# Optimization experiments

Measured on AMD Instinct MI355X. Metric: run time of the kernel, lower is better.

Reference implementation:

```python
import jax, jax.numpy as jnp
import numpy as np
import math

N_NODES = 100000
N_EDGES = 3200000
F_IN = 512
HID = 128
N_CLS = 16


def setup_inputs() -> dict:
    key = jax.random.key(0)
    k = jax.random.split(key, 6)
    x = jax.random.normal(k[0], (N_NODES, F_IN), dtype=jnp.float32)
    edge_index = jax.random.randint(k[1], (2, N_EDGES), 0, N_NODES, dtype=jnp.int32)
    W1 = jax.random.normal(k[2], (F_IN, HID), dtype=jnp.float32) / np.sqrt(F_IN)
    W2 = jax.random.normal(k[3], (HID, HID), dtype=jnp.float32) / np.sqrt(HID)
    W3 = jax.random.normal(k[4], (N_CLS, HID), dtype=jnp.float32) / np.sqrt(HID)
    b3 = jnp.zeros((N_CLS,), dtype=jnp.float32)
    return {"x": x, "edge_index": edge_index, "W1": W1, "W2": W2, "W3": W3, "b3": b3}


def _sym_norm(edge_index, num_nodes, dtype):
    # add self loops with fill_value = trunc(log2(average_node_degree))
    E = edge_index.shape[1]
    fill = float(math.trunc(math.log2(E / num_nodes)))
    loops = jnp.arange(num_nodes, dtype=edge_index.dtype)
    row = jnp.concatenate([edge_index[0], loops])
    col = jnp.concatenate([edge_index[1], loops])
    w = jnp.concatenate([jnp.ones((E,), dtype), jnp.full((num_nodes,), fill, dtype)])
    deg = jax.ops.segment_sum(w, row, num_segments=num_nodes)
    deg_inv_sqrt = jnp.where(deg > 0, jax.lax.rsqrt(deg), 0.0)
    norm = deg_inv_sqrt[row] * w * deg_inv_sqrt[col]
    return row, col, norm


def reference(x, edge_index, W1, W2, W3, b3):
    N = x.shape[0]
    row, col, norm = _sym_norm(edge_index, N, x.dtype)

    def gcn(h, W):
        h = h @ W                                   # [N, d_out]
        msg = norm[:, None] * h[col]                # gather + scale, [E', d_out]
        return jax.ops.segment_sum(msg, row, num_segments=N)

    h = jax.nn.relu(gcn(x, W1))      # layer 1 + srelu (threshold clamped at 0)
    h = gcn(h, W2)                   # layer 2
    # dropout p=0.5 is identity in eval mode
    return h @ W3.T + b3             # linear classifier [N, n_classes]
```

## Files before the change

kernel.cpp:

```cpp
#include <hip/hip_runtime.h>
#include <cmath>

typedef __attribute__((ext_vector_type(8))) short short8;
typedef __attribute__((ext_vector_type(8))) unsigned short ushort8;
typedef __attribute__((ext_vector_type(4))) float f32x4;
typedef __attribute__((ext_vector_type(4))) unsigned int uint4v;

#define EPB 4096

__device__ inline float bf16_lo(unsigned int p) {
  union { unsigned int i; float f; } v; v.i = p << 16; return v.f;
}
__device__ inline float bf16_hi(unsigned int p) {
  union { unsigned int i; float f; } v; v.i = p & 0xffff0000u; return v.f;
}
__device__ inline unsigned short f32_to_bf16(float f) {
  union { float f; unsigned int i; } v; v.f = f;
  unsigned int x = v.i;
  x += 0x7fffu + ((x >> 16) & 1u);
  return (unsigned short)(x >> 16);
}

__global__ __launch_bounds__(256) void bucket_hist2_k(const int* __restrict__ rows,
                                                      int* __restrict__ bucket_cnt, int E) {
  __shared__ int lh[256];
  const int t = threadIdx.x;
  lh[t] = 0;
  __syncthreads();
  const int base = blockIdx.x * EPB;
#pragma unroll
  for (int j = 0; j < 16; ++j) {
    int e = base + j * 256 + t;
    if (e < E) atomicAdd(&lh[rows[e] >> 9], 1);
  }
  __syncthreads();
  if (lh[t]) atomicAdd(&bucket_cnt[t], lh[t]);
}

__global__ void bucket_scan_k(const int* __restrict__ bucket_cnt,
                              int* __restrict__ bucket_base,
                              int* __restrict__ bucket_cursor,
                              int* __restrict__ row_ptr, int N, int Etot) {
  __shared__ int s[256];
  const int t = threadIdx.x;
  int v = bucket_cnt[t];
  s[t] = v;
  __syncthreads();
  for (int off = 1; off < 256; off <<= 1) {
    int add = (t >= off) ? s[t - off] : 0;
    __syncthreads();
    s[t] += add;
    __syncthreads();
  }
  int base = s[t] - v;
  bucket_base[t] = base;
  bucket_cursor[t] = base;
  if (t == 255) bucket_base[256] = s[255];
  if (t == 0) row_ptr[N] = Etot;
}

__global__ __launch_bounds__(256) void bin_k(const int* __restrict__ rows,
                                             const int* __restrict__ cols,
                                             int* __restrict__ bucket_cursor,
                                             unsigned int* __restrict__ binned, int E) {
  __shared__ int lhist[256];
  __shared__ int gbase[256];
  __shared__ int loff[256];
  const int t = threadIdx.x;
  const int base = blockIdx.x * EPB;
  lhist[t] = 0;
  __syncthreads();

  int bk[16];
  unsigned int pk[16];
#pragma unroll
  for (int j = 0; j < 16; ++j) {
    int e = base + j * 256 + t;
    if (e < E) {
      int r = rows[e];
      int c = cols[e];
      bk[j] = r >> 9;
      pk[j] = ((unsigned int)(r & 511) << 17) | (unsigned int)c;
      atomicAdd(&lhist[bk[j]], 1);
    } else {
      bk[j] = -1;
    }
  }
  __syncthreads();
  if (lhist[t] > 0) gbase[t] = atomicAdd(&bucket_cursor[t], lhist[t]);
  loff[t] = 0;
  __syncthreads();
#pragma unroll
  for (int j = 0; j < 16; ++j) {
    if (bk[j] >= 0) {
      int rank = atomicAdd(&loff[bk[j]], 1);
      binned[gbase[bk[j]] + rank] = pk[j];
    }
  }
}

__global__ __launch_bounds__(1024) void bucket_csr_k(const unsigned int* __restrict__ binned,
                                                     const int* __restrict__ bucket_base,
                                                     int* __restrict__ row_ptr,
                                                     float* __restrict__ dis,
                                                     int* __restrict__ col_sorted,
                                                     int N, float fill) {
  __shared__ int lcnt[512];
  __shared__ int lscan[512];
  const int b = blockIdx.x;
  const int t = threadIdx.x;
  const int start = bucket_base[b];
  const int endb = bucket_base[b + 1];
  const int rbase = b << 9;

  if (t < 512) lcnt[t] = 0;
  __syncthreads();
  for (int i = start + t; i < endb; i += 1024)
    atomicAdd(&lcnt[binned[i] >> 17], 1);
  __syncthreads();

  int v = (t < 512) ? lcnt[t] : 0;
  if (t < 512) lscan[t] = v;
  __syncthreads();
  for (int off = 1; off < 512; off <<= 1) {
    int add = (t < 512 && t >= off) ? lscan[t - off] : 0;
    __syncthreads();
    if (t < 512) lscan[t] += add;
    __syncthreads();
  }

  if (t < 512) {
    int excl = lscan[t] - v;
    int r = rbase + t;
    if (r < N) {
      row_ptr[r] = start + excl;
      float d = (float)v + fill;
      dis[r] = d > 0.f ? rsqrtf(d) : 0.f;
    }
    lcnt[t] = excl;
  }
  __syncthreads();

  for (int i = start + t; i < endb; i += 1024) {
    unsigned int pk = binned[i];
    int rl = (int)(pk >> 17);
    int c = (int)(pk & 0x1FFFFu);
    int pos = atomicAdd(&lcnt[rl], 1);
    col_sorted[start + pos] = c;
  }
}

__global__ __launch_bounds__(256) void cast_w_k(const float* __restrict__ W1,
                                                const float* __restrict__ W2,
                                                const float* __restrict__ W3,
                                                unsigned short* __restrict__ W1t,
                                                unsigned short* __restrict__ W2t,
                                                unsigned short* __restrict__ W3b,
                                                int FIN) {
  int g = blockIdx.x * 256 + threadIdx.x;
  int n1 = FIN * 128;
  if (g < n1) {
    int n = g & 127, k = g >> 7;
    W1t[n * FIN + k] = f32_to_bf16(W1[(size_t)k * 128 + n]);
  } else if (g < n1 + 128 * 128) {
    int gg = g - n1;
    int n = gg & 127, k = gg >> 7;
    W2t[n * 128 + k] = f32_to_bf16(W2[k * 128 + n]);
  } else if (g < n1 + 128 * 128 + 16 * 128) {
    int gg = g - n1 - 128 * 128;
    W3b[gg] = f32_to_bf16(W3[gg]);
  }
}

__global__ __launch_bounds__(256) void gemm_k(const void* __restrict__ Aq, int a_is_f32,
                                              int M, int K,
                                              const unsigned short* __restrict__ Bt,
                                              const float* __restrict__ dis,
                                              unsigned short* __restrict__ C) {
  __shared__ unsigned short Al[64 * 40];
  __shared__ unsigned short Bl[128 * 40];
  const int t = threadIdx.x;
  const int bm = blockIdx.x * 64;
  const int lane = t & 63;
  const int wave = t >> 6;
  const int wm = (wave >> 1) * 32;
  const int wn = (wave & 1) * 64;
  const int l15 = lane & 15;
  const int l4 = lane >> 4;

  f32x4 acc[2][4];
#pragma unroll
  for (int a = 0; a < 2; ++a)
#pragma unroll
    for (int b = 0; b < 4; ++b) acc[a][b] = (f32x4){0.f, 0.f, 0.f, 0.f};

  const int am = t >> 2;
  const int ak = (t & 3) * 8;
  const int bn = t >> 1;
  const int bk = (t & 1) * 16;
  const int arow = bm + am;

  for (int k0 = 0; k0 < K; k0 += 32) {
    ushort8 av = {0, 0, 0, 0, 0, 0, 0, 0};
    if (a_is_f32) {
      const float* A = (const float*)Aq;
      if (arow < M) {
        const float* p = A + (size_t)arow * K + k0 + ak;
#pragma unroll
        for (int j = 0; j < 8; ++j) av[j] = f32_to_bf16(p[j]);
      }
    } else {
      const unsigned short* A = (const unsigned short*)Aq;
      if (arow < M) av = *(const ushort8*)(A + (size_t)arow * K + k0 + ak);
    }
    ushort8 bv0 = *(const ushort8*)(Bt + (size_t)bn * K + k0 + bk);
    ushort8 bv1 = *(const ushort8*)(Bt + (size_t)bn * K + k0 + bk + 8);
    *(ushort8*)&Al[am * 40 + ak] = av;
    *(ushort8*)&Bl[bn * 40 + bk] = bv0;
    *(ushort8*)&Bl[bn * 40 + bk + 8] = bv1;
    __syncthreads();

    short8 a0 = *(const short8*)&Al[(wm + l15) * 40 + l4 * 8];
    short8 a1 = *(const short8*)&Al[(wm + 16 + l15) * 40 + l4 * 8];
#pragma unroll
    for (int nt = 0; nt < 4; ++nt) {
      short8 bfr = *(const short8*)&Bl[(wn + nt * 16 + l15) * 40 + l4 * 8];
      acc[0][nt] = __builtin_amdgcn_mfma_f32_16x16x32_bf16(a0, bfr, acc[0][nt], 0, 0, 0);
      acc[1][nt] = __builtin_amdgcn_mfma_f32_16x16x32_bf16(a1, bfr, acc[1][nt], 0, 0, 0);
    }
    __syncthreads();
  }

#pragma unroll
  for (int mt = 0; mt < 2; ++mt) {
    int rbase = bm + wm + mt * 16 + l4 * 4;
#pragma unroll
    for (int r = 0; r < 4; ++r) {
      int row = rbase + r;
      if (row < M) {
        float dr = dis[row];
#pragma unroll
        for (int nt = 0; nt < 4; ++nt) {
          int col = wn + nt * 16 + l15;
          C[(size_t)row * 128 + col] = f32_to_bf16(acc[mt][nt][r] * dr);
        }
      }
    }
  }
}

__global__ __launch_bounds__(256) void agg_k(const unsigned short* __restrict__ hs,
                                             const int* __restrict__ row_ptr,
                                             const int* __restrict__ cols,
                                             const float* __restrict__ dis,
                                             unsigned short* __restrict__ out,
                                             int N, float fill, int do_relu) {
  int r = blockIdx.x * 4 + (threadIdx.x >> 6);
  if (r >= N) return;
  const int lane = threadIdx.x & 63;
  const int sub = lane >> 4;
  const int fl = lane & 15;
  const uint4v* hv = (const uint4v*)hs;

  float a[8];
#pragma unroll
  for (int k = 0; k < 8; ++k) a[k] = 0.f;

  int e = row_ptr[r];
  const int end = row_ptr[r + 1];

  for (; e + 16 <= end; e += 16) {
    int c0 = cols[e + sub];
    int c1 = cols[e + 4 + sub];
    int c2 = cols[e + 8 + sub];
    int c3 = cols[e + 12 + sub];
    uint4v p0 = hv[(size_t)c0 * 16 + fl];
    uint4v p1 = hv[(size_t)c1 * 16 + fl];
    uint4v p2 = hv[(size_t)c2 * 16 + fl];
    uint4v p3 = hv[(size_t)c3 * 16 + fl];
#pragma unroll
    for (int k = 0; k < 4; ++k) {
      a[2 * k]     += bf16_lo(p0[k]) + bf16_lo(p1[k]);
      a[2 * k + 1] += bf16_hi(p0[k]) + bf16_hi(p1[k]);
      a[2 * k]     += bf16_lo(p2[k]) + bf16_lo(p3[k]);
      a[2 * k + 1] += bf16_hi(p2[k]) + bf16_hi(p3[k]);
    }
  }
  for (; e < end; e += 4) {
    int ee = e + sub;
    bool ok = ee < end;
    int c = ok ? cols[ee] : r;
    uint4v p = hv[(size_t)c * 16 + fl];
    if (!ok) p = (uint4v){0, 0, 0, 0};
#pragma unroll
    for (int k = 0; k < 4; ++k) {
      a[2 * k]     += bf16_lo(p[k]);
      a[2 * k + 1] += bf16_hi(p[k]);
    }
  }

#pragma unroll
  for (int k = 0; k < 8; ++k) {
    a[k] += __shfl_xor(a[k], 16);
    a[k] += __shfl_xor(a[k], 32);
  }

  if (sub == 0) {
    uint4v ps = hv[(size_t)r * 16 + fl];
    float dr = dis[r];
    uint4v o;
#pragma unroll
    for (int k = 0; k < 4; ++k) {
      float f0 = dr * (a[2 * k]     + fill * bf16_lo(ps[k]));
      float f1 = dr * (a[2 * k + 1] + fill * bf16_hi(ps[k]));
      if (do_relu) { f0 = fmaxf(f0, 0.f); f1 = fmaxf(f1, 0.f); }
      o[k] = ((unsigned int)f32_to_bf16(f1) << 16) | (unsigned int)f32_to_bf16(f0);
    }
    *((uint4v*)out + (size_t)r * 16 + fl) = o;
  }
}

__global__ __launch_bounds__(256) void fc_k(const unsigned short* __restrict__ h,
                                            const unsigned short* __restrict__ W3b,
                                            const float* __restrict__ b3,
                                            float* __restrict__ out, int N) {
  int g = blockIdx.x * 256 + threadIdx.x;
  if (g >= N * 16) return;
  int n = g >> 4, c = g & 15;
  const unsigned int* hv = (const unsigned int*)(h + (size_t)n * 128);
  const unsigned int* wv = (const unsigned int*)(W3b + c * 128);
  float acc = b3[c];
#pragma unroll 8
  for (int k = 0; k < 64; ++k) {
    unsigned int a = hv[k], w = wv[k];
    acc = fmaf(bf16_lo(a), bf16_lo(w), acc);
    acc = fmaf(bf16_hi(a), bf16_hi(w), acc);
  }
  out[g] = acc;
}

extern "C" void kernel_launch(void* const* d_in, const int* in_sizes, int n_in,
                              void* d_out, int out_size, void* d_ws, size_t ws_size,
                              hipStream_t stream) {
  const float* x  = (const float*)d_in[0];
  const int* edge = (const int*)d_in[1];
  const float* W1 = (const float*)d_in[2];
  const float* W2 = (const float*)d_in[3];
  const float* W3 = (const float*)d_in[4];
  const float* b3 = (const float*)d_in[5];
  float* out = (float*)d_out;

  const int HID = 128;
  const int FIN = in_sizes[2] / HID;
  const int N   = in_sizes[0] / FIN;
  const int E   = in_sizes[1] / 2;
  const float fill = truncf(log2f((float)E / (float)N));

  char* w = (char*)d_ws;
  size_t off = 0;
  auto alloc = [&](size_t bytes) -> void* {
    void* p = w + off;
    off += (bytes + 255) & ~(size_t)255;
    return p;
  };
  const int NB = (N + 511) >> 9;
  float* dis      = (float*)alloc((size_t)N * 4);
  int* row_ptr    = (int*)alloc(((size_t)N + 1) * 4);
  int* col_sorted = (int*)alloc((size_t)E * 4);
  int* bucket_cnt    = (int*)alloc(256 * 4);
  int* bucket_base   = (int*)alloc(257 * 4);
  int* bucket_cursor = (int*)alloc(256 * 4);
  unsigned int* binned = (unsigned int*)alloc((size_t)E * 4);
  unsigned short* W1t  = (unsigned short*)alloc((size_t)FIN * 128 * 2);
  unsigned short* W2t  = (unsigned short*)alloc(128 * 128 * 2);
  unsigned short* W3b  = (unsigned short*)alloc(16 * 128 * 2);
  unsigned short* bufA = (unsigned short*)alloc((size_t)N * 128 * 2);
  unsigned short* bufB = (unsigned short*)alloc((size_t)N * 128 * 2);

  const int* rows  = edge;
  const int* colsp = edge + E;

  hipMemsetAsync(bucket_cnt, 0, 256 * 4, stream);
  bucket_hist2_k<<<(E + EPB - 1) / EPB, 256, 0, stream>>>(rows, bucket_cnt, E);
  bucket_scan_k<<<1, 256, 0, stream>>>(bucket_cnt, bucket_base, bucket_cursor,
                                       row_ptr, N, E);
  bin_k<<<(E + EPB - 1) / EPB, 256, 0, stream>>>(rows, colsp, bucket_cursor, binned, E);
  bucket_csr_k<<<NB, 1024, 0, stream>>>(binned, bucket_base, row_ptr, dis,
                                        col_sorted, N, fill);
  const int castN = FIN * 128 + 128 * 128 + 16 * 128;
  cast_w_k<<<(castN + 255) / 256, 256, 0, stream>>>(W1, W2, W3, W1t, W2t, W3b, FIN);

  const int gm = (N + 63) / 64;
  gemm_k<<<gm, 256, 0, stream>>>(x, 1, N, FIN, W1t, dis, bufA);
  agg_k<<<(N + 3) / 4, 256, 0, stream>>>(bufA, row_ptr, col_sorted, dis, bufB, N, fill, 1);
  gemm_k<<<gm, 256, 0, stream>>>(bufB, 0, N, HID, W2t, dis, bufA);
  agg_k<<<(N + 3) / 4, 256, 0, stream>>>(bufA, row_ptr, col_sorted, dis, bufB, N, fill, 0);
  fc_k<<<(N * 16 + 255) / 256, 256, 0, stream>>>(bufB, W3b, b3, out, N);
}
```

Before: 696.3 us.

## Fuse classifier into second aggregation, prefetch GEMM tiles, widen gather unroll

Three changes. The final linear classifier moves into the second aggregation kernel's epilogue: each row's 128 features are dotted with the bf16 W3 in registers and reduced across 16 lanes with shuffles. This drops a kernel launch and the write and re-read of the hidden buffer. The GEMM now register-prefetches the next K tile's A and B values while the current tile is in LDS. The aggregation main loop now processes 32 edges per iteration instead of 16, with an 8-edge middle loop, which raises memory-level parallelism at some register cost.

```diff
diff --git a/kernel.cpp b/kernel.cpp
--- a/kernel.cpp
+++ b/kernel.cpp
@@ -13,6 +13,9 @@
 }
 __device__ inline float bf16_hi(unsigned int p) {
   union { unsigned int i; float f; } v; v.i = p & 0xffff0000u; return v.f;
+}
+__device__ inline float bf16u(unsigned short w) {
+  union { unsigned int i; float f; } v; v.i = (unsigned int)w << 16; return v.f;
 }
 __device__ inline unsigned short f32_to_bf16(float f) {
   union { float f; unsigned int i; } v; v.f = f;
@@ -199,26 +202,40 @@
   const int bn = t >> 1;
   const int bk = (t & 1) * 16;
   const int arow = bm + am;
-
-  for (int k0 = 0; k0 < K; k0 += 32) {
+  const bool arow_ok = arow < M;
+
+  auto load_a = [&](int k0) -> ushort8 {
     ushort8 av = {0, 0, 0, 0, 0, 0, 0, 0};
     if (a_is_f32) {
       const float* A = (const float*)Aq;
-      if (arow < M) {
+      if (arow_ok) {
         const float* p = A + (size_t)arow * K + k0 + ak;
 #pragma unroll
         for (int j = 0; j < 8; ++j) av[j] = f32_to_bf16(p[j]);
       }
     } else {
       const unsigned short* A = (const unsigned short*)Aq;
-      if (arow < M) av = *(const ushort8*)(A + (size_t)arow * K + k0 + ak);
-    }
-    ushort8 bv0 = *(const ushort8*)(Bt + (size_t)bn * K + k0 + bk);
-    ushort8 bv1 = *(const ushort8*)(Bt + (size_t)bn * K + k0 + bk + 8);
+      if (arow_ok) av = *(const ushort8*)(A + (size_t)arow * K + k0 + ak);
+    }
+    return av;
+  };
+
+  ushort8 av = load_a(0);
+  ushort8 bv0 = *(const ushort8*)(Bt + (size_t)bn * K + bk);
+  ushort8 bv1 = *(const ushort8*)(Bt + (size_t)bn * K + bk + 8);
+
+  for (int k0 = 0; k0 < K; k0 += 32) {
     *(ushort8*)&Al[am * 40 + ak] = av;
     *(ushort8*)&Bl[bn * 40 + bk] = bv0;
     *(ushort8*)&Bl[bn * 40 + bk + 8] = bv1;
     __syncthreads();
+
+    const int kn = k0 + 32;
+    if (kn < K) {
+      av = load_a(kn);
+      bv0 = *(const ushort8*)(Bt + (size_t)bn * K + kn + bk);
+      bv1 = *(const ushort8*)(Bt + (size_t)bn * K + kn + bk + 8);
+    }
 
     short8 a0 = *(const short8*)&Al[(wm + l15) * 40 + l4 * 8];
     short8 a1 = *(const short8*)&Al[(wm + 16 + l15) * 40 + l4 * 8];
@@ -253,8 +270,11 @@
                                              const int* __restrict__ row_ptr,
                                              const int* __restrict__ cols,
                                              const float* __restrict__ dis,
-                                             unsigned short* __restrict__ out,
-                                             int N, float fill, int do_relu) {
+                                             unsigned short* __restrict__ out_bf,
+                                             const unsigned short* __restrict__ W3b,
+                                             const float* __restrict__ b3,
+                                             float* __restrict__ fcout,
+                                             int N, float fill, int mode) {
   int r = blockIdx.x * 4 + (threadIdx.x >> 6);
   if (r >= N) return;
   const int lane = threadIdx.x & 63;
@@ -269,21 +289,40 @@
   int e = row_ptr[r];
   const int end = row_ptr[r + 1];
 
-  for (; e + 16 <= end; e += 16) {
+  for (; e + 32 <= end; e += 32) {
     int c0 = cols[e + sub];
     int c1 = cols[e + 4 + sub];
     int c2 = cols[e + 8 + sub];
     int c3 = cols[e + 12 + sub];
+    int c4 = cols[e + 16 + sub];
+    int c5 = cols[e + 20 + sub];
+    int c6 = cols[e + 24 + sub];
+    int c7 = cols[e + 28 + sub];
     uint4v p0 = hv[(size_t)c0 * 16 + fl];
     uint4v p1 = hv[(size_t)c1 * 16 + fl];
     uint4v p2 = hv[(size_t)c2 * 16 + fl];
     uint4v p3 = hv[(size_t)c3 * 16 + fl];
+    uint4v p4 = hv[(size_t)c4 * 16 + fl];
+    uint4v p5 = hv[(size_t)c5 * 16 + fl];
+    uint4v p6 = hv[(size_t)c6 * 16 + fl];
+    uint4v p7 = hv[(size_t)c7 * 16 + fl];
+#pragma unroll
+    for (int k = 0; k < 4; ++k) {
+      a[2 * k]     += (bf16_lo(p0[k]) + bf16_lo(p1[k])) + (bf16_lo(p2[k]) + bf16_lo(p3[k]))
+                    + (bf16_lo(p4[k]) + bf16_lo(p5[k])) + (bf16_lo(p6[k]) + bf16_lo(p7[k]));
+      a[2 * k + 1] += (bf16_hi(p0[k]) + bf16_hi(p1[k])) + (bf16_hi(p2[k]) + bf16_hi(p3[k]))
+                    + (bf16_hi(p4[k]) + bf16_hi(p5[k])) + (bf16_hi(p6[k]) + bf16_hi(p7[k]));
+    }
+  }
+  for (; e + 8 <= end; e += 8) {
+    int c0 = cols[e + sub];
+    int c1 = cols[e + 4 + sub];
+    uint4v p0 = hv[(size_t)c0 * 16 + fl];
+    uint4v p1 = hv[(size_t)c1 * 16 + fl];
 #pragma unroll
     for (int k = 0; k < 4; ++k) {
       a[2 * k]     += bf16_lo(p0[k]) + bf16_lo(p1[k]);
       a[2 * k + 1] += bf16_hi(p0[k]) + bf16_hi(p1[k]);
-      a[2 * k]     += bf16_lo(p2[k]) + bf16_lo(p3[k]);
-      a[2 * k + 1] += bf16_hi(p2[k]) + bf16_hi(p3[k]);
     }
   }
   for (; e < end; e += 4) {
@@ -308,35 +347,43 @@
   if (sub == 0) {
     uint4v ps = hv[(size_t)r * 16 + fl];
     float dr = dis[r];
-    uint4v o;
+    float v[8];
 #pragma unroll
     for (int k = 0; k < 4; ++k) {
-      float f0 = dr * (a[2 * k]     + fill * bf16_lo(ps[k]));
-      float f1 = dr * (a[2 * k + 1] + fill * bf16_hi(ps[k]));
-      if (do_relu) { f0 = fmaxf(f0, 0.f); f1 = fmaxf(f1, 0.f); }
-      o[k] = ((unsigned int)f32_to_bf16(f1) << 16) | (unsigned int)f32_to_bf16(f0);
-    }
-    *((uint4v*)out + (size_t)r * 16 + fl) = o;
-  }
-}
-
-__global__ __launch_bounds__(256) void fc_k(const unsigned short* __restrict__ h,
-                                            const unsigned short* __restrict__ W3b,
-                                            const float* __restrict__ b3,
-                                            float* __restrict__ out, int N) {
-  int g = blockIdx.x * 256 + threadIdx.x;
-  if (g >= N * 16) return;
-  int n = g >> 4, c = g & 15;
-  const unsigned int* hv = (const unsigned int*)(h + (size_t)n * 128);
-  const unsigned int* wv = (const unsigned int*)(W3b + c * 128);
-  float acc = b3[c];
-#pragma unroll 8
-  for (int k = 0; k < 64; ++k) {
-    unsigned int a = hv[k], w = wv[k];
-    acc = fmaf(bf16_lo(a), bf16_lo(w), acc);
-    acc = fmaf(bf16_hi(a), bf16_hi(w), acc);
-  }
-  out[g] = acc;
+      v[2 * k]     = dr * (a[2 * k]     + fill * bf16_lo(ps[k]));
+      v[2 * k + 1] = dr * (a[2 * k + 1] + fill * bf16_hi(ps[k]));
+    }
+    if (mode == 0) {
+      uint4v o;
+#pragma unroll
+      for (int k = 0; k < 4; ++k) {
+        float f0 = fmaxf(v[2 * k], 0.f);
+        float f1 = fmaxf(v[2 * k + 1], 0.f);
+        o[k] = ((unsigned int)f32_to_bf16(f1) << 16) | (unsigned int)f32_to_bf16(f0);
+      }
+      *((uint4v*)out_bf + (size_t)r * 16 + fl) = o;
+    } else {
+      float p[16];
+#pragma unroll
+      for (int c = 0; c < 16; ++c) {
+        ushort8 wr = *(const ushort8*)(W3b + c * 128 + fl * 8);
+        float s = v[0] * bf16u(wr[0]);
+        s = fmaf(v[1], bf16u(wr[1]), s);
+        s = fmaf(v[2], bf16u(wr[2]), s);
+        s = fmaf(v[3], bf16u(wr[3]), s);
+        s = fmaf(v[4], bf16u(wr[4]), s);
+        s = fmaf(v[5], bf16u(wr[5]), s);
+        s = fmaf(v[6], bf16u(wr[6]), s);
+        s = fmaf(v[7], bf16u(wr[7]), s);
+        p[c] = s;
+      }
+#pragma unroll
+      for (int m = 1; m <= 8; m <<= 1)
+#pragma unroll
+        for (int c = 0; c < 16; ++c) p[c] += __shfl_xor(p[c], m);
+      fcout[(size_t)r * 16 + fl] = p[fl] + b3[fl];
+    }
+  }
 }
 
 extern "C" void kernel_launch(void* const* d_in, const int* in_sizes, int n_in,
@@ -392,8 +439,9 @@
 
   const int gm = (N + 63) / 64;
   gemm_k<<<gm, 256, 0, stream>>>(x, 1, N, FIN, W1t, dis, bufA);
-  agg_k<<<(N + 3) / 4, 256, 0, stream>>>(bufA, row_ptr, col_sorted, dis, bufB, N, fill, 1);
+  agg_k<<<(N + 3) / 4, 256, 0, stream>>>(bufA, row_ptr, col_sorted, dis, bufB,
+                                         W3b, b3, out, N, fill, 0);
   gemm_k<<<gm, 256, 0, stream>>>(bufB, 0, N, HID, W2t, dis, bufA);
-  agg_k<<<(N + 3) / 4, 256, 0, stream>>>(bufA, row_ptr, col_sorted, dis, bufB, N, fill, 0);
-  fc_k<<<(N * 16 + 255) / 256, 256, 0, stream>>>(bufB, W3b, b3, out, N);
-}
+  agg_k<<<(N + 3) / 4, 256, 0, stream>>>(bufA, row_ptr, col_sorted, dis, bufB,
+                                         W3b, b3, out, N, fill, 1);
+}
```

After: 681.6 us. -2.1%, faster.
